# Kernel tuning notes

Measured on AMD Instinct MI355X. Metric: run time of the kernel, lower is better.

The kernel has to match this reference:

```python
import jax, jax.numpy as jnp
import numpy as np

B, N, D_IN = 16, 2048, 256
C, H = 32, 64          # num_capsules, dim_capsules
HEADS, KD = 4, 64      # attention heads, key_dim = dim_capsules
ROUTINGS = 3
EPS_SQ = 1e-7
LN_EPS = 1e-3


def squash(v, axis=-1):
    s2 = jnp.sum(jnp.square(v), axis=axis, keepdims=True)
    scale = s2 / (1.0 + s2) / jnp.sqrt(s2 + EPS_SQ)
    return scale * v


def setup_inputs() -> dict:
    key = jax.random.key(0)
    ks = jax.random.split(key, 10)
    # VarianceScaling(scale=2.0, fan_avg, uniform) for W
    fan_avg = (D_IN + H) / 2.0
    limit = float(np.sqrt(3.0 * 2.0 / fan_avg))
    W = jax.random.uniform(ks[0], (C, D_IN, H), minval=-limit, maxval=limit, dtype=jnp.float32)
    b_caps = jnp.zeros((C, H), jnp.float32)
    gamma = jnp.full((1,), 3.0, jnp.float32)
    x = jax.random.normal(ks[1], (B, N, D_IN), dtype=jnp.float32)
    def glorot(k, shape):
        fin, fout = shape[0], int(np.prod(shape[1:]))
        lim = float(np.sqrt(6.0 / (fin + fout)))
        return jax.random.uniform(k, shape, minval=-lim, maxval=lim, dtype=jnp.float32)
    Wq = glorot(ks[2], (H, HEADS, KD)); bq = jnp.zeros((HEADS, KD), jnp.float32)
    Wk = glorot(ks[3], (H, HEADS, KD)); bk = jnp.zeros((HEADS, KD), jnp.float32)
    Wv = glorot(ks[4], (H, HEADS, KD)); bv = jnp.zeros((HEADS, KD), jnp.float32)
    Wo = glorot(ks[5], (HEADS, KD, H)); bo = jnp.zeros((H,), jnp.float32)
    ln_gamma = jnp.ones((H,), jnp.float32)
    ln_beta = jnp.zeros((H,), jnp.float32)
    return dict(x=x, W=W, b_caps=b_caps, gamma=gamma,
                Wq=Wq, bq=bq, Wk=Wk, bk=bk, Wv=Wv, bv=bv, Wo=Wo, bo=bo,
                ln_gamma=ln_gamma, ln_beta=ln_beta)


def dynamic_routing(u_hat):
    # u_hat: [B, N, C, H]
    b = jnp.zeros(u_hat.shape[:3] + (1,), u_hat.dtype)
    v = None
    for i in range(ROUTINGS):
        c = jax.nn.softmax(b, axis=2)                      # [B,N,C,1]
        s = jnp.sum(c * u_hat, axis=1, keepdims=True)      # [B,1,C,H]
        v = squash(s, axis=-1)
        if i < ROUTINGS - 1:
            agreement = jnp.sum(u_hat * v, axis=-1, keepdims=True)
            b = b + agreement
    return jnp.squeeze(v, axis=1)                          # [B,C,H]


def mha_self(xq, Wq, bq, Wk, bk, Wv, bv, Wo, bo):
    # xq: [B, C, H]
    q = jnp.einsum('bch,hnk->bcnk', xq, Wq) + bq
    k = jnp.einsum('bch,hnk->bcnk', xq, Wk) + bk
    v = jnp.einsum('bch,hnk->bcnk', xq, Wv) + bv
    scores = jnp.einsum('bqnd,bknd->bnqk', q, k) / jnp.sqrt(jnp.asarray(KD, xq.dtype))
    attn = jax.nn.softmax(scores, axis=-1)
    ctx = jnp.einsum('bnqk,bknd->bqnd', attn, v)
    return jnp.einsum('bqnd,ndh->bqh', ctx, Wo) + bo


def reference(x, W, b_caps, gamma, Wq, bq, Wk, bk, Wv, bv, Wo, bo, ln_gamma, ln_beta):
    u_hat = jnp.einsum('bnd,cdh->bnch', x, W) + b_caps[None, None]  # [B,N,C,H]
    routed = dynamic_routing(u_hat)                                  # [B,C,H]
    attended = mha_self(routed, Wq, bq, Wk, bk, Wv, bv, Wo, bo)
    y = attended + routed
    mu = jnp.mean(y, axis=-1, keepdims=True)
    var = jnp.mean(jnp.square(y - mu), axis=-1, keepdims=True)
    routed = (y - mu) / jnp.sqrt(var + LN_EPS) * ln_gamma + ln_beta
    return squash(routed, axis=-1) * gamma
```

## Files before the change

kernel.cpp:

```cpp
#include <hip/hip_runtime.h>
#include <cstddef>

typedef _Float16 f16;
typedef __attribute__((ext_vector_type(8))) _Float16 f16x8;
typedef __attribute__((ext_vector_type(4))) float f32x4;

namespace {
constexpr int kB = 16;
constexpr int kN = 2048;
constexpr int kD = 256;
constexpr int kC = 32;
constexpr int kH = 64;
constexpr int kHeads = 4;
constexpr int kKD = 64;
constexpr int kChunks = 32;
constexpr int kRows = kN / kChunks;

constexpr size_t OFF_XPART = 0;
constexpr size_t OFF_V     = OFF_XPART + 65536;
constexpr size_t OFF_WV    = OFF_V + 32768;
constexpr size_t OFF_BV    = OFF_WV + 131072;
constexpr size_t OFF_Y     = OFF_BV + 512;
constexpr size_t OFF_CS    = OFF_Y + 131072;
constexpr size_t OFF_CTX   = OFF_CS + 512;
constexpr size_t OFF_XF16  = OFF_CTX + 524288;
constexpr size_t OFF_WVH   = OFF_XF16 + 4194304;
constexpr size_t OFF_CSP   = OFF_WVH + 65536;
constexpr size_t OFF_YP    = OFF_CSP + 16384;
constexpr size_t WS_NEED_PARTIAL = (OFF_YP + 4194304) * sizeof(float);
}

__global__ __launch_bounds__(256) void k_xpart(const float* __restrict__ x,
                                               float* __restrict__ xpart,
                                               f16* __restrict__ xh) {
  const int b = blockIdx.x, j = blockIdx.y, d = threadIdx.x;
  const size_t base = ((size_t)b * kN + (size_t)j * 128) * kD + d;
  const float* xp = x + base;
  f16* xo = xh + base;
  float s = 0.f;
#pragma unroll 4
  for (int n = 0; n < 128; ++n) {
    const float v = xp[(size_t)n * kD];
    s += v;
    xo[(size_t)n * kD] = (f16)v;
  }
  xpart[((size_t)b * 16 + j) * kD + d] = s;
}

__global__ __launch_bounds__(256) void k_sv(
    const float* __restrict__ W, const float* __restrict__ b_caps,
    const float* __restrict__ xpart, const float* __restrict__ y,
    const float* __restrict__ csum, const float* __restrict__ ypart,
    const float* __restrict__ cspart, float* __restrict__ v,
    float* __restrict__ Wv, f16* __restrict__ Wvh, float* __restrict__ bv,
    const int mode, const int computeWv, const int accWv, const int npart) {
  const int bc = blockIdx.x, b = bc >> 5, c = bc & 31;
  const int t = threadIdx.x;
  const int w = t >> 6, h = t & 63;
  __shared__ float yL[kD];
  __shared__ float sL[4][kH];
  __shared__ float vL[kH];
  __shared__ float csLs;

  if (mode == 0) {
    float s = 0.f;
#pragma unroll
    for (int j = 0; j < 16; ++j) s += xpart[((size_t)b * 16 + j) * kD + t];
    yL[t] = s * (1.f / (float)kC);
    if (t == 0) csLs = (float)kN / (float)kC;
  } else if (npart > 0) {
    float s = 0.f;
#pragma unroll 8
    for (int ch = 0; ch < kChunks; ++ch)
      s += ypart[(((size_t)b * kChunks + ch) * kC + c) * kD + t];
    yL[t] = s;
    if (t < 32) {
      float cs_ = cspart[((size_t)b * kChunks + t) * kC + c];
#pragma unroll
      for (int off = 16; off; off >>= 1) cs_ += __shfl_xor(cs_, off, 64);
      if (t == 0) csLs = cs_;
    }
  } else {
    yL[t] = y[(size_t)bc * kD + t];
    if (t == 0) csLs = csum[bc];
  }
  __syncthreads();

  const float* Wc = W + (size_t)c * kD * kH;
  {
    float acc = 0.f;
#pragma unroll 8
    for (int d = w * 64; d < (w + 1) * 64; ++d)
      acc = fmaf(yL[d], Wc[(size_t)d * kH + h], acc);
    sL[w][h] = acc;
  }
  __syncthreads();

  if (t < 64) {
    const float bch = b_caps[c * kH + h];
    float s = sL[0][h] + sL[1][h] + sL[2][h] + sL[3][h] + csLs * bch;
    float s2 = s * s;
#pragma unroll
    for (int off = 32; off; off >>= 1) s2 += __shfl_xor(s2, off, 64);
    const float scale = s2 / (1.f + s2) * rsqrtf(s2 + 1e-7f);
    const float vh = scale * s;
    v[(size_t)bc * kH + h] = vh;
    vL[h] = vh;
    if (computeWv) {
      float bvp = bch * vh;
#pragma unroll
      for (int off = 32; off; off >>= 1) bvp += __shfl_xor(bvp, off, 64);
      if (h == 0) bv[bc] = accWv ? (bv[bc] + bvp) : bvp;
    }
  }
  __syncthreads();
  if (computeWv) {
    float acc = 0.f;
    const float* Wrow = Wc + (size_t)t * kH;
#pragma unroll 8
    for (int hh = 0; hh < kH; ++hh) acc = fmaf(Wrow[hh], vL[hh], acc);
    const size_t idx = (size_t)bc * kD + t;
    const float nv = accWv ? (Wv[idx] + acc) : acc;
    Wv[idx] = nv;
    Wvh[idx] = (f16)nv;
  }
}

__global__ __launch_bounds__(256) void k_route(
    const f16* __restrict__ xh, const f16* __restrict__ Wvh,
    const float* __restrict__ bv, float* __restrict__ y,
    float* __restrict__ csum, float* __restrict__ ypart,
    float* __restrict__ cspart, const int usePart) {
  const int b = blockIdx.x, chunk = blockIdx.y;
  const int t = threadIdx.x;
  const int lane = t & 63, w = t >> 6;
  const int l15 = lane & 15, q = lane >> 4;

  __shared__ __align__(16) f16 xsT[kD][kRows + 8];
  __shared__ float aL[kRows][kC + 1];
  __shared__ __align__(16) f16 pT[kC][kRows + 8];
  __shared__ float csL[8][kC];

  const int n0 = chunk * kRows;
  const float bvc = bv[b * kC + (t & 31)];

  {
    const int r = lane, d0 = w * 64;
    const f16x8* gs = reinterpret_cast<const f16x8*>(
        xh + ((size_t)(b * kN + n0 + r)) * kD + d0);
#pragma unroll
    for (int jj = 0; jj < 8; ++jj) {
      f16x8 vv = gs[jj];
#pragma unroll
      for (int i = 0; i < 8; ++i) xsT[d0 + jj * 8 + i][r] = vv[i];
    }
  }

  f32x4 acc0 = {0.f, 0.f, 0.f, 0.f}, acc1 = {0.f, 0.f, 0.f, 0.f};
  {
    const f16x8* Ar = reinterpret_cast<const f16x8*>(
        xh + ((size_t)(b * kN + n0 + w * 16 + l15)) * kD + q * 8);
    const f16x8* B0 = reinterpret_cast<const f16x8*>(
        Wvh + ((size_t)(b * kC + l15)) * kD + q * 8);
    const f16x8* B1 = reinterpret_cast<const f16x8*>(
        Wvh + ((size_t)(b * kC + 16 + l15)) * kD + q * 8);
#pragma unroll
    for (int ks = 0; ks < 8; ++ks) {
      f16x8 af = Ar[ks * 4];
      acc0 = __builtin_amdgcn_mfma_f32_16x16x32_f16(af, B0[ks * 4], acc0, 0, 0, 0);
      acc1 = __builtin_amdgcn_mfma_f32_16x16x32_f16(af, B1[ks * 4], acc1, 0, 0, 0);
    }
  }
#pragma unroll
  for (int r = 0; r < 4; ++r) {
    aL[w * 16 + q * 4 + r][l15] = acc0[r];
    aL[w * 16 + q * 4 + r][16 + l15] = acc1[r];
  }
  __syncthreads();

  const int c = t & 31, sg = t >> 5;
  float csreg = 0.f;
#pragma unroll
  for (int k = 0; k < 8; ++k) {
    const int r = sg * 8 + k;
    float L = bvc + aL[r][c];
    float m = L;
#pragma unroll
    for (int off = 16; off; off >>= 1) m = fmaxf(m, __shfl_xor(m, off, 64));
    const float e = __expf(L - m);
    float ssum = e;
#pragma unroll
    for (int off = 16; off; off >>= 1) ssum += __shfl_xor(ssum, off, 64);
    const float p = e / ssum;
    pT[c][r] = (f16)p;
    csreg += p;
  }
  csL[sg][c] = csreg;
  __syncthreads();

  const int mt2 = w & 1;
  const int ntb = (w >> 1) * 8;
  const f16x8 a0 = *reinterpret_cast<const f16x8*>(&pT[mt2 * 16 + l15][q * 8]);
  const f16x8 a1 = *reinterpret_cast<const f16x8*>(&pT[mt2 * 16 + l15][32 + q * 8]);
  const int cap = mt2 * 16 + q * 4;
#pragma unroll
  for (int i = 0; i < 8; ++i) {
    const int d0 = (ntb + i) * 16;
    const f16x8 b0 = *reinterpret_cast<const f16x8*>(&xsT[d0 + l15][q * 8]);
    const f16x8 b1 = *reinterpret_cast<const f16x8*>(&xsT[d0 + l15][32 + q * 8]);
    f32x4 o = {0.f, 0.f, 0.f, 0.f};
    o = __builtin_amdgcn_mfma_f32_16x16x32_f16(a0, b0, o, 0, 0, 0);
    o = __builtin_amdgcn_mfma_f32_16x16x32_f16(a1, b1, o, 0, 0, 0);
    if (usePart) {
      float* dst = ypart + (((size_t)(b * kChunks + chunk)) * kC + cap) * kD + d0 + l15;
#pragma unroll
      for (int r = 0; r < 4; ++r) dst[(size_t)r * kD] = o[r];
    } else {
      float* dst = y + ((size_t)(b * kC + cap)) * kD + d0 + l15;
#pragma unroll
      for (int r = 0; r < 4; ++r) atomicAdd(dst + (size_t)r * kD, o[r]);
    }
  }
  if (t < 32) {
    float s = 0.f;
#pragma unroll
    for (int j = 0; j < 8; ++j) s += csL[j][t];
    if (usePart) cspart[((size_t)b * kChunks + chunk) * kC + t] = s;
    else atomicAdd(csum + b * kC + t, s);
  }
}

__global__ __launch_bounds__(256) void k_mha2(
    const float* __restrict__ routed, const float* __restrict__ Wq,
    const float* __restrict__ bq, const float* __restrict__ Wk,
    const float* __restrict__ bk, const float* __restrict__ Wvp,
    const float* __restrict__ bvp, float* __restrict__ ctx) {
  const int b = blockIdx.x, head = blockIdx.y, t = threadIdx.x;
  __shared__ float rL[kC * kH];
  __shared__ float WqL[kH][kKD + 1];
  __shared__ float WkL[kH][kKD + 1];
  __shared__ float WvL[kH][kKD + 1];
  __shared__ float qL[kC][kKD];
  __shared__ float kL[kC][kKD + 1];
  __shared__ float vL[kC][kKD];
  __shared__ float sc[kC][kC + 1];
#pragma unroll
  for (int i = 0; i < 8; ++i) rL[t + 256 * i] = routed[(size_t)b * kC * kH + t + 256 * i];
#pragma unroll
  for (int i = 0; i < 16; ++i) {
    const int e = t + 256 * i, hh = e >> 6, kk = e & 63;
    const size_t wi = ((size_t)hh * kHeads + head) * kKD + kk;
    WqL[hh][kk] = Wq[wi];
    WkL[hh][kk] = Wk[wi];
    WvL[hh][kk] = Wvp[wi];
  }
  __syncthreads();
#pragma unroll
  for (int i = 0; i < 8; ++i) {
    const int e = t + 256 * i, cc = e >> 6, kk = e & 63;
    float aq = bq[head * kKD + kk];
    float ak = bk[head * kKD + kk];
    float av = bvp[head * kKD + kk];
#pragma unroll 8
    for (int hh = 0; hh < kH; ++hh) {
      const float r = rL[cc * kH + hh];
      aq = fmaf(r, WqL[hh][kk], aq);
      ak = fmaf(r, WkL[hh][kk], ak);
      av = fmaf(r, WvL[hh][kk], av);
    }
    qL[cc][kk] = aq; kL[cc][kk] = ak; vL[cc][kk] = av;
  }
  __syncthreads();
#pragma unroll
  for (int i = 0; i < 4; ++i) {
    const int e = t + 256 * i, qc = e >> 5, kc = e & 31;
    float s = 0.f;
#pragma unroll 8
    for (int d = 0; d < kKD; ++d) s = fmaf(qL[qc][d], kL[kc][d], s);
    sc[qc][kc] = s * 0.125f;
  }
  __syncthreads();
  if (t < kC) {
    float m = -1e30f;
#pragma unroll
    for (int kc = 0; kc < kC; ++kc) m = fmaxf(m, sc[t][kc]);
    float ssum = 0.f;
#pragma unroll
    for (int kc = 0; kc < kC; ++kc) {
      const float e2 = __expf(sc[t][kc] - m);
      sc[t][kc] = e2;
      ssum += e2;
    }
    const float inv = 1.f / ssum;
#pragma unroll
    for (int kc = 0; kc < kC; ++kc) sc[t][kc] *= inv;
  }
  __syncthreads();
#pragma unroll
  for (int i = 0; i < 8; ++i) {
    const int e = t + 256 * i, qc = e >> 6, d = e & 63;
    float s = 0.f;
#pragma unroll 8
    for (int kc = 0; kc < kC; ++kc) s = fmaf(sc[qc][kc], vL[kc][d], s);
    ctx[(((size_t)b * kC + qc) * kHeads + head) * kKD + d] = s;
  }
}

__global__ __launch_bounds__(256) void k_final(
    const float* __restrict__ ctx, const float* __restrict__ Wo,
    const float* __restrict__ bo, const float* __restrict__ routed,
    const float* __restrict__ ln_g, const float* __restrict__ ln_b,
    const float* __restrict__ gamma, float* __restrict__ out) {
  const int bc = blockIdx.x, t = threadIdx.x;
  const int w = t >> 6, h = t & 63;
  __shared__ float cL[kHeads * kKD];
  __shared__ float sL[4][kH];
  cL[t] = ctx[(size_t)bc * (kHeads * kKD) + t];
  __syncthreads();
  float acc = 0.f;
#pragma unroll 8
  for (int nd = w * 64; nd < (w + 1) * 64; ++nd)
    acc = fmaf(cL[nd], Wo[(size_t)nd * kH + h], acc);
  sL[w][h] = acc;
  __syncthreads();
  if (t < 64) {
    const float yv = sL[0][h] + sL[1][h] + sL[2][h] + sL[3][h] + bo[h] +
                     routed[(size_t)bc * kH + h];
    float mu = yv;
#pragma unroll
    for (int off = 32; off; off >>= 1) mu += __shfl_xor(mu, off, 64);
    mu *= (1.f / (float)kH);
    const float dv = yv - mu;
    float var = dv * dv;
#pragma unroll
    for (int off = 32; off; off >>= 1) var += __shfl_xor(var, off, 64);
    var *= (1.f / (float)kH);
    const float nrm = dv * rsqrtf(var + 1e-3f) * ln_g[h] + ln_b[h];
    float s2 = nrm * nrm;
#pragma unroll
    for (int off = 32; off; off >>= 1) s2 += __shfl_xor(s2, off, 64);
    const float scale = s2 / (1.f + s2) * rsqrtf(s2 + 1e-7f);
    out[(size_t)bc * kH + h] = scale * nrm * gamma[0];
  }
}

extern "C" void kernel_launch(void* const* d_in, const int* in_sizes, int n_in,
                              void* d_out, int out_size, void* d_ws, size_t ws_size,
                              hipStream_t stream) {
  (void)in_sizes; (void)n_in; (void)out_size;
  const float* x      = (const float*)d_in[0];
  const float* W      = (const float*)d_in[1];
  const float* b_caps = (const float*)d_in[2];
  const float* gamma  = (const float*)d_in[3];
  const float* Wq     = (const float*)d_in[4];
  const float* bq     = (const float*)d_in[5];
  const float* Wk     = (const float*)d_in[6];
  const float* bk     = (const float*)d_in[7];
  const float* Wv_in  = (const float*)d_in[8];
  const float* bv_in  = (const float*)d_in[9];
  const float* Wo     = (const float*)d_in[10];
  const float* bo     = (const float*)d_in[11];
  const float* ln_g   = (const float*)d_in[12];
  const float* ln_b   = (const float*)d_in[13];
  float* out = (float*)d_out;
  float* ws  = (float*)d_ws;

  float* xpart = ws + OFF_XPART;
  float* v     = ws + OFF_V;
  float* Wv    = ws + OFF_WV;
  float* bv    = ws + OFF_BV;
  float* y     = ws + OFF_Y;
  float* cs    = ws + OFF_CS;
  float* ctx   = ws + OFF_CTX;
  f16*   xf16  = (f16*)(ws + OFF_XF16);
  f16*   wvh   = (f16*)(ws + OFF_WVH);
  float* csp   = ws + OFF_CSP;
  float* yp    = ws + OFF_YP;

  const int usePart = (ws_size >= WS_NEED_PARTIAL) ? 1 : 0;

  k_xpart<<<dim3(kB, 16), 256, 0, stream>>>(x, xpart, xf16);
  k_sv<<<kB * kC, 256, 0, stream>>>(W, b_caps, xpart, y, cs, yp, csp, v, Wv, wvh, bv,
                                    0, 1, 0, 0);

  if (!usePart) {
    hipMemsetAsync(y, 0, (size_t)kB * kC * kD * sizeof(float), stream);
    hipMemsetAsync(cs, 0, (size_t)kB * kC * sizeof(float), stream);
  }
  k_route<<<dim3(kB, kChunks), 256, 0, stream>>>(xf16, wvh, bv, y, cs, yp, csp, usePart);
  k_sv<<<kB * kC, 256, 0, stream>>>(W, b_caps, xpart, y, cs, yp, csp, v, Wv, wvh, bv,
                                    1, 1, 1,
                                    usePart ? kChunks : 0);

  if (!usePart) {
    hipMemsetAsync(y, 0, (size_t)kB * kC * kD * sizeof(float), stream);
    hipMemsetAsync(cs, 0, (size_t)kB * kC * sizeof(float), stream);
  }
  k_route<<<dim3(kB, kChunks), 256, 0, stream>>>(xf16, wvh, bv, y, cs, yp, csp, usePart);
  k_sv<<<kB * kC, 256, 0, stream>>>(W, b_caps, xpart, y, cs, yp, csp, v, Wv, wvh, bv,
                                    1, 0, 0,
                                    usePart ? kChunks : 0);

  k_mha2<<<dim3(kB, kHeads), 256, 0, stream>>>(v, Wq, bq, Wk, bk, Wv_in, bv_in, ctx);
  k_final<<<kB * kC, 256, 0, stream>>>(ctx, Wo, bo, v, ln_g, ln_b, gamma, out);
}
```

Baseline: 189.2 us.

## Widen xpart grid, fuse xsT transpose into MFMA loads, split MHA into qkv and attention

```diff
diff --git a/kernel.cpp b/kernel.cpp
--- a/kernel.cpp
+++ b/kernel.cpp
@@ -15,14 +15,16 @@
 constexpr int kKD = 64;
 constexpr int kChunks = 32;
 constexpr int kRows = kN / kChunks;
+constexpr int kXJ = 64;
 
 constexpr size_t OFF_XPART = 0;
-constexpr size_t OFF_V     = OFF_XPART + 65536;
+constexpr size_t OFF_V     = OFF_XPART + 262144;
 constexpr size_t OFF_WV    = OFF_V + 32768;
 constexpr size_t OFF_BV    = OFF_WV + 131072;
 constexpr size_t OFF_Y     = OFF_BV + 512;
 constexpr size_t OFF_CS    = OFF_Y + 131072;
-constexpr size_t OFF_CTX   = OFF_CS + 512;
+constexpr size_t OFF_QKV   = OFF_CS + 512;
+constexpr size_t OFF_CTX   = OFF_QKV + 393216;
 constexpr size_t OFF_XF16  = OFF_CTX + 524288;
 constexpr size_t OFF_WVH   = OFF_XF16 + 4194304;
 constexpr size_t OFF_CSP   = OFF_WVH + 65536;
@@ -34,17 +36,17 @@
                                                float* __restrict__ xpart,
                                                f16* __restrict__ xh) {
   const int b = blockIdx.x, j = blockIdx.y, d = threadIdx.x;
-  const size_t base = ((size_t)b * kN + (size_t)j * 128) * kD + d;
+  const size_t base = ((size_t)b * kN + (size_t)j * 32) * kD + d;
   const float* xp = x + base;
   f16* xo = xh + base;
   float s = 0.f;
-#pragma unroll 4
-  for (int n = 0; n < 128; ++n) {
+#pragma unroll
+  for (int n = 0; n < 32; ++n) {
     const float v = xp[(size_t)n * kD];
     s += v;
     xo[(size_t)n * kD] = (f16)v;
   }
-  xpart[((size_t)b * 16 + j) * kD + d] = s;
+  xpart[((size_t)b * kXJ + j) * kD + d] = s;
 }
 
 __global__ __launch_bounds__(256) void k_sv(
@@ -64,8 +66,8 @@
 
   if (mode == 0) {
     float s = 0.f;
-#pragma unroll
-    for (int j = 0; j < 16; ++j) s += xpart[((size_t)b * 16 + j) * kD + t];
+#pragma unroll 8
+    for (int j = 0; j < kXJ; ++j) s += xpart[((size_t)b * kXJ + j) * kD + t];
     yL[t] = s * (1.f / (float)kC);
     if (t == 0) csLs = (float)kN / (float)kC;
   } else if (npart > 0) {
@@ -137,29 +139,18 @@
   const int l15 = lane & 15, q = lane >> 4;
 
   __shared__ __align__(16) f16 xsT[kD][kRows + 8];
-  __shared__ float aL[kRows][kC + 1];
+  __shared__ float aL[kRows][kC + 4];
   __shared__ __align__(16) f16 pT[kC][kRows + 8];
   __shared__ float csL[8][kC];
 
   const int n0 = chunk * kRows;
   const float bvc = bv[b * kC + (t & 31)];
 
-  {
-    const int r = lane, d0 = w * 64;
-    const f16x8* gs = reinterpret_cast<const f16x8*>(
-        xh + ((size_t)(b * kN + n0 + r)) * kD + d0);
-#pragma unroll
-    for (int jj = 0; jj < 8; ++jj) {
-      f16x8 vv = gs[jj];
-#pragma unroll
-      for (int i = 0; i < 8; ++i) xsT[d0 + jj * 8 + i][r] = vv[i];
-    }
-  }
-
   f32x4 acc0 = {0.f, 0.f, 0.f, 0.f}, acc1 = {0.f, 0.f, 0.f, 0.f};
   {
+    const int row = w * 16 + l15;
     const f16x8* Ar = reinterpret_cast<const f16x8*>(
-        xh + ((size_t)(b * kN + n0 + w * 16 + l15)) * kD + q * 8);
+        xh + ((size_t)(b * kN + n0 + row)) * kD + q * 8);
     const f16x8* B0 = reinterpret_cast<const f16x8*>(
         Wvh + ((size_t)(b * kC + l15)) * kD + q * 8);
     const f16x8* B1 = reinterpret_cast<const f16x8*>(
@@ -169,6 +160,12 @@
       f16x8 af = Ar[ks * 4];
       acc0 = __builtin_amdgcn_mfma_f32_16x16x32_f16(af, B0[ks * 4], acc0, 0, 0, 0);
       acc1 = __builtin_amdgcn_mfma_f32_16x16x32_f16(af, B1[ks * 4], acc1, 0, 0, 0);
+      const int dbase = ks * 32 + q * 8;
+#pragma unroll
+      for (int i = 0; i < 8; ++i) {
+        const int ii = (i + 2 * q) & 7;
+        xsT[dbase + ii][row] = af[ii];
+      }
     }
   }
 #pragma unroll
@@ -230,45 +227,53 @@
   }
 }
 
-__global__ __launch_bounds__(256) void k_mha2(
+__global__ __launch_bounds__(256) void k_qkv(
     const float* __restrict__ routed, const float* __restrict__ Wq,
     const float* __restrict__ bq, const float* __restrict__ Wk,
     const float* __restrict__ bk, const float* __restrict__ Wvp,
-    const float* __restrict__ bvp, float* __restrict__ ctx) {
+    const float* __restrict__ bvp, float* __restrict__ qkv) {
+  const int b = blockIdx.x, head = blockIdx.y, which = blockIdx.z;
+  const int t = threadIdx.x;
+  const int kk = t & 63, w = t >> 6;
+  const float* Wsrc = (which == 0) ? Wq : (which == 1) ? Wk : Wvp;
+  const float* bsrc = (which == 0) ? bq : (which == 1) ? bk : bvp;
+  __shared__ float rL[kC * kH];
+#pragma unroll
+  for (int i = 0; i < 8; ++i) rL[t + 256 * i] = routed[(size_t)b * kC * kH + t + 256 * i];
+  __syncthreads();
+  float acc[8];
+  const float bb = bsrc[head * kKD + kk];
+#pragma unroll
+  for (int i = 0; i < 8; ++i) acc[i] = bb;
+#pragma unroll 4
+  for (int hh = 0; hh < kH; ++hh) {
+    const float wv = Wsrc[((size_t)hh * kHeads + head) * kKD + kk];
+#pragma unroll
+    for (int i = 0; i < 8; ++i)
+      acc[i] = fmaf(rL[(w + 4 * i) * kH + hh], wv, acc[i]);
+  }
+#pragma unroll
+  for (int i = 0; i < 8; ++i) {
+    const int cc = w + 4 * i;
+    qkv[((((size_t)which * kB + b) * kHeads + head) * kC + cc) * kKD + kk] = acc[i];
+  }
+}
+
+__global__ __launch_bounds__(256) void k_attn2(const float* __restrict__ qkv,
+                                               float* __restrict__ ctx) {
   const int b = blockIdx.x, head = blockIdx.y, t = threadIdx.x;
-  __shared__ float rL[kC * kH];
-  __shared__ float WqL[kH][kKD + 1];
-  __shared__ float WkL[kH][kKD + 1];
-  __shared__ float WvL[kH][kKD + 1];
+  constexpr size_t kWhichStride = (size_t)kB * kHeads * kC * kKD;
+  const size_t base = ((size_t)b * kHeads + head) * kC * kKD;
   __shared__ float qL[kC][kKD];
   __shared__ float kL[kC][kKD + 1];
   __shared__ float vL[kC][kKD];
   __shared__ float sc[kC][kC + 1];
 #pragma unroll
-  for (int i = 0; i < 8; ++i) rL[t + 256 * i] = routed[(size_t)b * kC * kH + t + 256 * i];
-#pragma unroll
-  for (int i = 0; i < 16; ++i) {
-    const int e = t + 256 * i, hh = e >> 6, kk = e & 63;
-    const size_t wi = ((size_t)hh * kHeads + head) * kKD + kk;
-    WqL[hh][kk] = Wq[wi];
-    WkL[hh][kk] = Wk[wi];
-    WvL[hh][kk] = Wvp[wi];
-  }
-  __syncthreads();
-#pragma unroll
   for (int i = 0; i < 8; ++i) {
     const int e = t + 256 * i, cc = e >> 6, kk = e & 63;
-    float aq = bq[head * kKD + kk];
-    float ak = bk[head * kKD + kk];
-    float av = bvp[head * kKD + kk];
-#pragma unroll 8
-    for (int hh = 0; hh < kH; ++hh) {
-      const float r = rL[cc * kH + hh];
-      aq = fmaf(r, WqL[hh][kk], aq);
-      ak = fmaf(r, WkL[hh][kk], ak);
-      av = fmaf(r, WvL[hh][kk], av);
-    }
-    qL[cc][kk] = aq; kL[cc][kk] = ak; vL[cc][kk] = av;
+    qL[cc][kk] = qkv[base + e];
+    kL[cc][kk] = qkv[base + kWhichStride + e];
+    vL[cc][kk] = qkv[base + 2 * kWhichStride + e];
   }
   __syncthreads();
 #pragma unroll
@@ -371,6 +376,7 @@
   float* bv    = ws + OFF_BV;
   float* y     = ws + OFF_Y;
   float* cs    = ws + OFF_CS;
+  float* qkv   = ws + OFF_QKV;
   float* ctx   = ws + OFF_CTX;
   f16*   xf16  = (f16*)(ws + OFF_XF16);
   f16*   wvh   = (f16*)(ws + OFF_WVH);
@@ -379,7 +385,7 @@
 
   const int usePart = (ws_size >= WS_NEED_PARTIAL) ? 1 : 0;
 
-  k_xpart<<<dim3(kB, 16), 256, 0, stream>>>(x, xpart, xf16);
+  k_xpart<<<dim3(kB, kXJ), 256, 0, stream>>>(x, xpart, xf16);
   k_sv<<<kB * kC, 256, 0, stream>>>(W, b_caps, xpart, y, cs, yp, csp, v, Wv, wvh, bv,
                                     0, 1, 0, 0);
 
@@ -401,6 +407,7 @@
                                     1, 0, 0,
                                     usePart ? kChunks : 0);
 
-  k_mha2<<<dim3(kB, kHeads), 256, 0, stream>>>(v, Wq, bq, Wk, bk, Wv_in, bv_in, ctx);
+  k_qkv<<<dim3(kB, kHeads, 3), 256, 0, stream>>>(v, Wq, bq, Wk, bk, Wv_in, bv_in, qkv);
+  k_attn2<<<dim3(kB, kHeads), 256, 0, stream>>>(qkv, ctx);
   k_final<<<kB * kC, 256, 0, stream>>>(ctx, Wo, bo, v, ln_g, ln_b, gamma, out);
 }
```

Result: faster. 179.0 us (-5.4%).
